# Kernel optimization log

Hardware: AMD Instinct MI355X
Metric: run time of the kernel (lower is better)

## Reference

```python
import jax, jax.numpy as jnp
import numpy as np
from jax import lax
from jax.scipy.linalg import cho_solve, solve_triangular

T_LEN, D, K = 8192, 32, 16
LOG2PI = float(np.log(2.0 * np.pi))


def setup_inputs():
    ks = jax.random.split(jax.random.key(0), 14)
    R = 0.1 * jax.random.normal(ks[0], (T_LEN, D, D))
    recog_J = jnp.einsum('tij,tkj->tik', R, R) + 0.5 * jnp.eye(D)  # SPD recognition precisions
    recog_h = 0.1 * jax.random.normal(ks[1], (T_LEN, D, 1))
    loc = 0.1 * jax.random.normal(ks[2], (D, 1))
    Tau_p = jnp.eye(D) + 0.05 * jax.random.normal(ks[3], (D, D))
    Lambda_p = jnp.eye(D) + 0.05 * jax.random.normal(ks[4], (D, D))
    X = 0.9 * jnp.eye(D, D + 1) + 0.05 * jax.random.normal(ks[5], (D, D + 1))
    init_lps = jax.nn.log_softmax(jax.random.normal(ks[6], (K,)))[:, None]
    trans_lps = jax.nn.log_softmax(jax.random.normal(ks[7], (K, K)), axis=1)
    Rp = 0.1 * jax.random.normal(ks[8], (K, D, D))
    prior_lam = jnp.einsum('kij,klj->kil', Rp, Rp) + jnp.eye(D)
    prior_X = 0.9 * jnp.eye(D, D + 1) + 0.05 * jax.random.normal(ks[9], (K, D, D + 1))
    Rt = 0.1 * jax.random.normal(ks[10], (D, D))
    prior_tau = Rt @ Rt.T + jnp.eye(D)
    prior_mu = 0.1 * jax.random.normal(ks[11], (D, 1))
    init_lps_prior = jax.nn.log_softmax(jax.random.normal(ks[12], (K,)))[:, None]
    trans_lps_prior = jax.nn.log_softmax(jax.random.normal(ks[13], (K, K)), axis=1)
    return dict(recog_J=recog_J, recog_h=recog_h, loc=loc, Tau_p=Tau_p, Lambda_p=Lambda_p, X=X,
                init_lps=init_lps, trans_lps=trans_lps, prior_lam=prior_lam, prior_X=prior_X,
                prior_tau=prior_tau, prior_mu=prior_mu, init_lps_prior=init_lps_prior,
                trans_lps_prior=trans_lps_prior, seed=42)


def _slds(recog_J, recog_h, loc, Tau_p, Lambda_p, X, init_lps, trans_lps,
          prior_lam, prior_X, prior_tau, prior_mu, init_lps_prior, trans_lps_prior, seed):
    Dd = loc.shape[0]
    Kk = init_lps.shape[0]
    Tt = recog_J.shape[0]
    Nn = Tt - 1
    eye = jnp.eye(Dd, dtype=recog_J.dtype)
    jitter = 1e-6 * eye

    # expected_params: inference LDS natural params
    tau = Tau_p @ Tau_p.T + 1e-8 * eye
    tau_mu = tau @ loc
    lam = Lambda_p @ Lambda_p.T + 1e-8 * eye
    A = X[:, :Dd]
    b = X[:, Dd:]
    ATlam = A.T @ lam
    ATlamA = ATlam @ A
    lamA = lam @ A
    lamb = lam @ b
    ATlamb = A.T @ lamb
    bTlamb = (b.T @ lamb)[0, 0]
    logdet_lam = jnp.linalg.slogdet(lam)[1]

    # ---- HMM forward-backward over z_{1:N} (emissions are zeros, kept general) ----
    emit = jnp.zeros((Nn, Kk), dtype=recog_J.dtype)

    def fstep(a, e):
        a2 = jax.nn.logsumexp(a[:, None] + trans_lps, axis=0) + e
        return a2, a2
    a0 = init_lps[:, 0] + emit[0]
    _, alphas_rest = lax.scan(fstep, a0, emit[1:])
    alphas = jnp.concatenate([a0[None], alphas_rest], 0)  # (N,K)
    hmm_logZ = jax.nn.logsumexp(alphas[-1])

    def bstep(beta_next, e_next):
        beta = jax.nn.logsumexp(trans_lps + (e_next + beta_next)[None, :], axis=1)
        return beta, beta
    _, betas_head = lax.scan(bstep, jnp.zeros(Kk, dtype=recog_J.dtype), emit[1:], reverse=True)
    betas = jnp.concatenate([betas_head, jnp.zeros((1, Kk), dtype=recog_J.dtype)], 0)
    cat_es = jnp.exp(alphas + betas - hmm_logZ)  # (N,K) marginals q(z_t)
    pair = jnp.exp(alphas[:-1, :, None] + trans_lps[None] + (emit[1:] + betas[1:])[:, None, :] - hmm_logZ)
    EZZNT = jnp.sum(pair, 0)  # (K,K) expected transition counts

    hmm_kl = (jnp.sum(cat_es[0] * (init_lps[:, 0] - init_lps_prior[:, 0]))
              + jnp.sum(EZZNT * (trans_lps - trans_lps_prior))
              + jnp.sum(cat_es * emit) - hmm_logZ)

    # ---- LDS information-form Kalman filter (computes logZ of q) ----
    J0 = tau + recog_J[0]
    h0 = tau_mu + recog_h[0]
    logc0 = -0.5 * (loc.T @ tau_mu)[0, 0] + 0.5 * jnp.linalg.slogdet(tau)[1] - 0.5 * Dd * LOG2PI

    def filt(carry, xs):
        J, h, lc = carry
        Jr, hr = xs
        M = J + ATlamA + jitter
        C = jnp.linalg.cholesky(M)
        u = h - ATlamb
        Minv_u = cho_solve((C, True), u)
        logdetM = 2.0 * jnp.sum(jnp.log(jnp.diagonal(C)))
        Jn = lam + Jr - lamA @ cho_solve((C, True), ATlam)
        hn = lamb + hr + lamA @ Minv_u
        lc = lc - 0.5 * bTlamb + 0.5 * logdet_lam + 0.5 * (u.T @ Minv_u)[0, 0] - 0.5 * logdetM
        return (Jn, hn, lc), (Jn, hn)

    (Jlast, hlast, logc), (Jf_rest, hf_rest) = lax.scan(filt, (J0, h0, logc0), (recog_J[1:], recog_h[1:]))
    Jf = jnp.concatenate([J0[None], Jf_rest], 0)  # (T,D,D) filtered precisions
    hf = jnp.concatenate([h0[None], hf_rest], 0)  # (T,D,1)
    Cl = jnp.linalg.cholesky(Jlast + jitter)
    mlast = cho_solve((Cl, True), hlast)
    logZq = logc + 0.5 * (hlast.T @ mlast)[0, 0] + 0.5 * Dd * LOG2PI - jnp.sum(jnp.log(jnp.diagonal(Cl)))

    # ---- RTS smoother -> gaussian expected stats ----
    CovT = cho_solve((Cl, True), eye)

    def smooth(carry, xs):
        m_n, Cov_n = carry
        Jt, ht = xs
        P = Jt + ATlamA + jitter
        C = jnp.linalg.cholesky(P)
        G = cho_solve((C, True), ATlam)
        g = cho_solve((C, True), ht - ATlamb)
        m = G @ m_n + g
        Pinv = cho_solve((C, True), eye)
        Cov = Pinv + G @ Cov_n @ G.T
        cross = G @ (Cov_n + m_n @ m_n.T) + g @ m_n.T  # E[x_t x_{t+1}^T]
        return (m, Cov), (m, Cov, cross)

    _, (m_head, Cov_head, cross) = lax.scan(smooth, (mlast, CovT), (Jf[:-1], hf[:-1]), reverse=True)
    Ex = jnp.concatenate([m_head, mlast[None]], 0)  # (T,D,1)
    Cov = jnp.concatenate([Cov_head, CovT[None]], 0)
    ExxT = Cov + jnp.einsum('tiz,tjz->tij', Ex, Ex)  # (T,D,D)
    Cross = jnp.swapaxes(cross, 1, 2)  # E[x_{t+1} x_t^T], (N,D,D)
    Ex2 = Ex[..., 0]

    # ---- E_q[log p_inf(x)] ----
    init_term = (-0.5 * jnp.einsum('ij,ij->', tau, ExxT[0]) + jnp.dot(Ex2[0], tau_mu[:, 0])
                 - 0.5 * (loc.T @ tau_mu)[0, 0] + 0.5 * jnp.linalg.slogdet(tau)[1] - 0.5 * Dd * LOG2PI)
    trans_term = (-0.5 * jnp.einsum('ij,nij->', lam, ExxT[1:])
                  + jnp.einsum('ij,nij->', lamA, Cross)
                  - 0.5 * jnp.einsum('ij,nij->', ATlamA, ExxT[:-1])
                  + jnp.einsum('i,ni->', lamb[:, 0], Ex2[1:])
                  - jnp.einsum('i,ni->', ATlamb[:, 0], Ex2[:-1])
                  + Nn * (-0.5 * bTlamb + 0.5 * logdet_lam - 0.5 * Dd * LOG2PI))
    E_log_p_inf = init_term + trans_term

    # ---- hmm_to_lds_mf: mixture (mean-field) prior expected log-density ----
    Ak = prior_X[:, :, :Dd]
    bk = prior_X[:, :, Dd:]
    lamAk = jnp.einsum('kij,kjl->kil', prior_lam, Ak)
    ATlamAk = jnp.einsum('kji,kjl->kil', Ak, lamAk)
    lambk = jnp.einsum('kij,kjz->kiz', prior_lam, bk)
    ATlambk = jnp.einsum('kji,kjz->kiz', Ak, lambk)
    bTlambk = jnp.einsum('kjz,kjz->k', bk, lambk)
    logdetk = jnp.linalg.slogdet(prior_lam)[1]
    w = cat_es  # (N,K)
    mix_trans = (-0.5 * jnp.einsum('nk,kij,nij->', w, prior_lam, ExxT[1:])
                 + jnp.einsum('nk,kij,nij->', w, lamAk, Cross)
                 - 0.5 * jnp.einsum('nk,kij,nij->', w, ATlamAk, ExxT[:-1])
                 + jnp.einsum('nk,ki,ni->', w, lambk[:, :, 0], Ex2[1:])
                 - jnp.einsum('nk,ki,ni->', w, ATlambk[:, :, 0], Ex2[:-1])
                 + jnp.einsum('nk,k->', w, -0.5 * bTlambk + 0.5 * logdetk)
                 - 0.5 * Nn * Dd * LOG2PI)
    tpm = prior_tau @ prior_mu
    mix_init = (-0.5 * jnp.einsum('ij,ij->', prior_tau, ExxT[0]) + jnp.dot(Ex2[0], tpm[:, 0])
                - 0.5 * (prior_mu.T @ tpm)[0, 0] + 0.5 * jnp.linalg.slogdet(prior_tau)[1] - 0.5 * Dd * LOG2PI)
    E_log_p_mix = mix_init + mix_trans

    recog_term = (-0.5 * jnp.einsum('tij,tij->', recog_J, ExxT)
                  + jnp.einsum('tiz,tiz->', recog_h, Ex))
    lds_kl = E_log_p_inf + recog_term - logZq - E_log_p_mix

    # ---- joint backward sampling of x_{1:T} ~ q ----
    eps = jax.random.normal(jax.random.fold_in(jax.random.key(seed), 1), (Tt, Dd, 1), dtype=recog_J.dtype)
    xT = mlast + solve_triangular(Cl.T, eps[-1], lower=False)

    def samp(x_next, xs):
        Jt, ht, e = xs
        P = Jt + ATlamA + jitter
        C = jnp.linalg.cholesky(P)
        mean = cho_solve((C, True), ht - ATlamb + ATlam @ x_next)
        x = mean + solve_triangular(C.T, e, lower=False)
        return x, x

    _, xs_head = lax.scan(samp, xT, (Jf[:-1], hf[:-1], eps[:-1]), reverse=True)
    z = jnp.concatenate([xs_head, xT[None]], 0)[..., 0]  # (T,D)

    return z, Ex, ExxT, Cross, cat_es, lds_kl + hmm_kl


def reference(recog_J, recog_h, loc, Tau_p, Lambda_p, X, init_lps, trans_lps,
              prior_lam, prior_X, prior_tau, prior_mu, init_lps_prior, trans_lps_prior, seed):
    return _slds(recog_J, recog_h, loc, Tau_p, Lambda_p, X, init_lps, trans_lps,
                 prior_lam, prior_X, prior_tau, prior_mu, init_lps_prior, trans_lps_prior, seed)
```

## Files before the change

kernel.cpp:

```cpp
#include <hip/hip_runtime.h>
#include <math.h>
#include <stdint.h>

#define Dd 32
#define TT 8192
#define NN 8191
#define KK 16
#define LOG2PI_ 1.8378770664093453

#define WSD_LOGC0  0
#define WSD_LOGZQ  1
#define WSD_MIXC   3
#define WSD_LDLAM  4
#define WSD_BTLAMB 5
#define WSD_PR     8
#define WSD_PT     1032
#define WSD_PM     2056
#define F_TAU      0
#define F_TAUMU    1024
#define F_LAM      1056
#define F_A        2080
#define F_B        3104
#define F_ATLAM    3136
#define F_ATLAMA   4160
// ... 121 lines not shown
  dst[(j0+2)*36+m]=v.z; dst[(j0+3)*36+m]=v.w;
}
__device__ __forceinline__ void t36_sym(float* dst, const float* packed, int tid){
  for(int q=tid;q<528;q+=256){
    int r,c; tri_rc(q,r,c);
    float v=packed[q];
    dst[r*36+c]=v; dst[c*36+r]=v;
  }
}

__device__ double chol_linv36(float* W, float* Li, float* rdg, int tid){
  int r = tid>>3, c0 = (tid&7)<<2;
  {
    float4 z = make_float4(0.f,0.f,0.f,0.f);
    if(r>=c0 && r<c0+4) ((float*)&z)[r-c0]=1.f;
    *(float4*)(Li + r*36 + c0) = z;
  }
  double slog=0.0;
  for(int j=0;j<33;++j){
    if(j<32){
      float dd = W[j*36+j];
      float rd = 1.0f/sqrtf(dd);
      float invd = rd*rd;
      if(tid==0){ rdg[j]=rd; slog += (double)(0.5f*__logf(dd)); }
      if(r>j && c0+3>=j){
        float t0 = W[j*36+r]*invd;
        float4 wj  = *(const float4*)(W+j*36+c0);
        float4 cur = *(float4*)(W+r*36+c0);
        float rdl = rd;
        int c;
        c=c0;   cur.x = (c>j)? fmaf(-t0, wj.x, cur.x) : ((c==j)? cur.x*rdl : cur.x);
        c=c0+1; cur.y = (c>j)? fmaf(-t0, wj.y, cur.y) : ((c==j)? cur.y*rdl : cur.y);
        c=c0+2; cur.z = (c>j)? fmaf(-t0, wj.z, cur.z) : ((c==j)? cur.z*rdl : cur.z);
        c=c0+3; cur.w = (c>j)? fmaf(-t0, wj.w, cur.w) : ((c==j)? cur.w*rdl : cur.w);
        *(float4*)(W+r*36+c0) = cur;
      }
    }
    if(j>0){
      int ii=j-1;
      if(r>ii && c0<=ii){
        float wri = W[r*36+ii]*rdg[ii];
        float4 lrow = *(const float4*)(Li+ii*36+c0);
        float4 cur  = *(float4*)(Li+r*36+c0);
        if(c0+0<=ii) cur.x = fmaf(-wri, lrow.x, cur.x);
        if(c0+1<=ii) cur.y = fmaf(-wri, lrow.y, cur.y);
        if(c0+2<=ii) cur.z = fmaf(-wri, lrow.z, cur.z);
        if(c0+3<=ii) cur.w = fmaf(-wri, lrow.w, cur.w);
        *(float4*)(Li+r*36+c0) = cur;
      }
    }
    __syncthreads();
  }
  {
    float rr = rdg[r];
    float4 cur = *(float4*)(Li+r*36+c0);
    cur.x*=rr; cur.y*=rr; cur.z*=rr; cur.w*=rr;
    *(float4*)(Li+r*36+c0) = cur;
  }
  __syncthreads();
  return slog;
}

__device__ __forceinline__ double blk_red(double v, double* sd, int tid){
  sd[tid]=v; __syncthreads();
  for(int s=128;s>0;s>>=1){ if(tid<s) sd[tid]+=sd[tid+s]; __syncthreads(); }
  double r=sd[0]; __syncthreads(); return r;
}
__device__ double blk_logdet(float* Ms, int tid){
  double sl = 0.0;
  for (int j=0;j<Dd;++j){
    float dd = Ms[j*33+j];
    sl += log((double)dd);
    float invd = 1.0f/dd;
    #pragma unroll
    for(int p=0;p<4;p++){
      int cell = tid + (p<<8); int r=cell>>5, c=cell&31;
      if(r>j && c>j && c<=r) Ms[r*33+c] -= Ms[r*33+j]*(Ms[c*33+j]*invd);
    }
    __syncthreads();
  }
  return sl;
}

__global__ __launch_bounds__(256) void k_setup(const float* rJ, const float* rh, const float* loc,
    const float* Tp, const float* Lp, const float* X, const float* plam, const float* pX,
    const float* ptau, const float* pmu, float* wsf, double* wsd){
  __shared__ float s1[1056], s2[1056], s3[1056];
  __shared__ float sv[32], sv2[32];
  int tid=threadIdx.x; int b=blockIdx.x;
  if(b==0){
    for(int p=0;p<4;p++){int cell=tid+(p<<8);int r=cell>>5,c=cell&31; s1[r*33+c]=Tp[cell];}
    if(tid<32) sv[tid]=loc[tid];
    __syncthreads();
    for(int p=0;p<4;p++){int cell=tid+(p<<8);int r=cell>>5,c=cell&31;
      float a=0.f;
      #pragma unroll
      for(int m=0;m<Dd;++m) a=fmaf(s1[r*33+m], s1[c*33+m], a);
      if(r==c) a+=1e-8f;
      s2[r*33+c]=a; wsf[F_TAU+cell]=a; wsf[F_J0+cell]=a+rJ[cell];
    }
    __syncthreads();
    if(tid<32){ float tm=0.f;
      #pragma unroll
      for(int m=0;m<Dd;++m) tm=fmaf(s2[tid*33+m], sv[m], tm);
      sv2[tid]=tm; wsf[F_TAUMU+tid]=tm; wsf[F_H0+tid]=tm+rh[tid];
    }
    __syncthreads();
    double ldt = blk_logdet(s2, tid);
    if(tid==0){ double dd=0; for(int m=0;m<Dd;++m) dd += (double)sv[m]*(double)sv2[m];
      wsd[WSD_LOGC0] = -0.5*dd + 0.5*ldt - 0.5*Dd*LOG2PI_; }
  } else if(b==1){
    for(int p=0;p<4;p++){int cell=tid+(p<<8);int r=cell>>5,c=cell&31; s1[r*33+c]=Lp[cell];}
    __syncthreads();
    for(int p=0;p<4;p++){int cell=tid+(p<<8);int r=cell>>5,c=cell&31;
      float a=0.f;
      #pragma unroll
      for(int m=0;m<Dd;++m) a=fmaf(s1[r*33+m], s1[c*33+m], a);
      if(r==c) a+=1e-8f;
      s2[r*33+c]=a; wsf[F_LAM+cell]=a;
    }
    __syncthreads();
    for(int p=0;p<4;p++){int cell=tid+(p<<8);int r=cell>>5,c=cell&31;
      float a=X[r*33+c]; s3[r*33+c]=a; wsf[F_A+cell]=a; }
    if(tid<32){ sv[tid]=X[tid*33+32]; wsf[F_B+tid]=sv[tid]; }
    __syncthreads();
    for(int p=0;p<4;p++){int cell=tid+(p<<8);int r=cell>>5,c=cell&31;
      float a=0.f,b2=0.f;
      #pragma unroll
      for(int m=0;m<Dd;++m){ a=fmaf(s2[r*33+m], s3[m*33+c], a); b2=fmaf(s3[m*33+r], s2[m*33+c], b2); }
      s1[r*33+c]=a; wsf[F_LAMA+cell]=a; wsf[F_ATLAM+cell]=b2;
    }
    if(tid<32){ float lb=0.f;
      #pragma unroll
      for(int m=0;m<Dd;++m) lb=fmaf(s2[tid*33+m], sv[m], lb);
      sv2[tid]=lb; wsf[F_LAMB+tid]=lb;
    }
    __syncthreads();
    for(int p=0;p<4;p++){int cell=tid+(p<<8);int r=cell>>5,c=cell&31;
      float a=0.f;
      #pragma unroll
      for(int m=0;m<Dd;++m) a=fmaf(s3[m*33+r], s1[m*33+c], a);
      wsf[F_ATLAMA+cell]=a;
    }
    if(tid<32){ float ab=0.f;
      #pragma unroll
      for(int m=0;m<Dd;++m) ab=fmaf(s3[m*33+tid], sv2[m], ab);
      wsf[F_ATLAMB+tid]=ab;
    }
    if(tid==0){ double bb=0; for(int m=0;m<Dd;++m) bb += (double)sv[m]*(double)sv2[m];
      wsd[WSD_BTLAMB]=bb; }
    __syncthreads();
    double ldl = blk_logdet(s2, tid);
    if(tid==0) wsd[WSD_LDLAM]=ldl;
  } else if(b==2){
    for(int p=0;p<4;p++){int cell=tid+(p<<8);int r=cell>>5,c=cell&31; s1[r*33+c]=ptau[cell];}
    if(tid<32) sv[tid]=pmu[tid];
    __syncthreads();
    if(tid<32){ float tm=0.f;
      #pragma unroll
      for(int m=0;m<Dd;++m) tm=fmaf(s1[tid*33+m], sv[m], tm);
      sv2[tid]=tm; wsf[F_TPM+tid]=tm;
    }
    __syncthreads();
    double ldp = blk_logdet(s1, tid);
    if(tid==0){ double dd=0; for(int m=0;m<Dd;++m) dd += (double)sv[m]*(double)sv2[m];
      wsd[WSD_MIXC] = -0.5*dd + 0.5*ldp - 0.5*Dd*LOG2PI_; }
// ... 68 lines not shown

__global__ __launch_bounds__(256) void k_hmmab(const float* il, float* wsf){
  __shared__ float S[3328];
  int tid=threadIdx.x;
  for(int p=0;p<13;++p) S[p*256+tid]=wsf[F_TPOW+p*256+tid];
  __syncthreads();
  int n = blockIdx.x*256 + tid;
  if(n>NN-1) return;
  float v[16], w[16];
  #pragma unroll
  for(int j=0;j<16;++j) v[j]=il[j];
  for(int k=0;k<13;++k){
    if((n>>k)&1){
      #pragma unroll
      for(int j=0;j<16;++j){
        float mx=-3.0e38f;
        #pragma unroll
        for(int i2=0;i2<16;++i2) mx=fmaxf(mx, v[i2]+S[k*256+i2*16+j]);
        float s=0.f;
        #pragma unroll
        for(int i2=0;i2<16;++i2) s+=__expf(v[i2]+S[k*256+i2*16+j]-mx);
        w[j]=mx+__logf(s);
      }
      #pragma unroll
      for(int j=0;j<16;++j) v[j]=w[j];
    }
  }
  #pragma unroll
  for(int j=0;j<16;++j) wsf[F_ALPHA+(size_t)n*16+j]=v[j];
  if(n==NN-1){
    float mx=-3.0e38f;
    #pragma unroll
    for(int j=0;j<16;++j) mx=fmaxf(mx,v[j]);
    float s=0.f;
    #pragma unroll
    for(int j=0;j<16;++j) s+=__expf(v[j]-mx);
    wsf[F_SC+0]=mx+__logf(s);
  }
  int m = NN-1-n;
  float b[16];
  #pragma unroll
  for(int i2=0;i2<16;++i2) b[i2]=0.f;
  for(int k=0;k<13;++k){
    if((m>>k)&1){
      #pragma unroll
      for(int i2=0;i2<16;++i2){
        float mx=-3.0e38f;
        #pragma unroll
        for(int j=0;j<16;++j) mx=fmaxf(mx, S[k*256+i2*16+j]+b[j]);
        float s=0.f;
        #pragma unroll
        for(int j=0;j<16;++j) s+=__expf(S[k*256+i2*16+j]+b[j]-mx);
        w[i2]=mx+__logf(s);
      }
      #pragma unroll
      for(int i2=0;i2<16;++i2) b[i2]=w[i2];
    }
  }
  #pragma unroll
  for(int i2=0;i2<16;++i2) wsf[F_BETA+(size_t)n*16+i2]=b[i2];
}

__global__ __launch_bounds__(256) void k_cat(const float* tl, float* wsf, float* out){
  __shared__ float Ts[256]; __shared__ float al[1024]; __shared__ float be[1040];
  int tid=threadIdx.x;
  Ts[tid]=tl[tid];
  float logZ = wsf[F_SC+0];
  int n0=blockIdx.x*64;
  for(int q=tid;q<1024;q+=256){ int n=n0+(q>>4); al[q] = (n<NN)? wsf[F_ALPHA+(size_t)n*16+(q&15)] : 0.f; }
  for(int q=tid;q<1040;q+=256){ int n=n0+(q>>4); be[q] = (n<NN)? wsf[F_BETA +(size_t)n*16+(q&15)] : 0.f; }
  __syncthreads();
  for(int q=tid;q<1024;q+=256){ int n=n0+(q>>4);
    if(n<NN) out[O_CAT+(size_t)n*16+(q&15)] = __expf(al[q]+be[q]-logZ); }
  int i=tid>>4, j=tid&15;
  float acc=0.f;
  #pragma unroll 4
  for(int nn=0;nn<64;++nn){
    int n=n0+nn;
    if(n<NN-1) acc += __expf(al[nn*16+i]+Ts[i*16+j]+be[(nn+1)*16+j]-logZ);
  }
  wsf[F_EZ + blockIdx.x*256 + tid]=acc;
}

__global__ __launch_bounds__(256) void k_leaf(const float* rJ, const float* rh, float* wsf, double* wsd){
  int b = blockIdx.x; int tid=threadIdx.x;
  float* pe = wsf + F_SCAN + (size_t)b*SSTR;
  if(b==0){
    for(int q=tid;q<528;q+=256){
      int r,c; tri_rc(q,r,c);
      pe[POFF+q]=0.f;
      pe[QOFF+q]=wsf[F_J0 + r*32+c];
    }
    for(int q=tid;q<1024;q+=256) pe[ROFF+q]=0.f;
    if(tid<32){ pe[PPOFF+tid]=0.f; pe[QQOFF+tid]=wsf[F_H0+tid]; }
    if(tid==0){ *(double*)(pe+GAMOFF)=wsd[WSD_LOGC0]; pe[FLGOFF]=1.f; }
  } else {
    int t = b;
    for(int q=tid;q<528;q+=256){
      int r,c; tri_rc(q,r,c);
      pe[POFF+q] = wsf[F_ATLAMA + r*32+c] + ((r==c)?1e-6f:0.f);
      pe[QOFF+q] = wsf[F_LAM + r*32+c] + rJ[(size_t)t*1024 + r*32+c];
    }
    for(int q=tid;q<1024;q+=256) pe[ROFF+q] = -wsf[F_ATLAM+q];
    if(tid<32){
      pe[PPOFF+tid] = -wsf[F_ATLAMB+tid];
      pe[QQOFF+tid] = wsf[F_LAMB+tid] + rh[(size_t)t*32+tid];
    }
    if(tid==0){
      *(double*)(pe+GAMOFF) = -0.5*wsd[WSD_BTLAMB] + 0.5*wsd[WSD_LDLAM];
      pe[FLGOFF]=1.f;
    }
  }
}

__global__ __launch_bounds__(256) void k_cf(float* wsf, float* out, int d, int mode){
  __shared__ __align__(16) float SA[2148], SB[2148];
  __shared__ __align__(16) float W[1152], Li[1152], BA[1152], BB[1152];
  __shared__ float rdg[32], Ls[32];
  int tid = threadIdx.x;
  int i = blockIdx.x;
  int iA = (i<<(d+1)) + (1<<d) - 1;
  int iB = iA + (1<<d);
  float* base = wsf + F_SCAN;
  float* pa = base + (size_t)iA*SSTR;
  float* pb = base + (size_t)iB*SSTR;
  for(int q=tid;q<537;q+=256){ ((float4*)SA)[q]=((const float4*)pa)[q]; ((float4*)SB)[q]=((const float4*)pb)[q]; }
  __syncthreads();
  int fa=(SA[FLGOFF]!=0.f), fb=(SB[FLGOFF]!=0.f);
  if(mode==1){
    float* st = out + O_EXXT;
    for(int q=tid;q<537;q+=256){ ((float4*)st)[q]=((float4*)SB)[q]; ((float4*)pb)[q]=((float4*)SA)[q]; }
    if(tid==0) pa[FLGOFF]=0.f;
    return;
  }
  if(mode==2){ for(int q=tid;q<537;q+=256) ((float4*)pa)[q]=((float4*)SB)[q]; }
  float* X = (mode==2)? SB : SA;  int fx=(mode==2)?fb:fa;
  float* Y = (mode==2)? SA : SB;  int fy=(mode==2)?fa:fb;
  if(!fx && !fy){ if(tid==0) pb[FLGOFF]=0.f; return; }
  if(!fx){ for(int q=tid;q<537;q+=256) ((float4*)pb)[q]=((float4*)Y)[q]; return; }
  if(!fy){ for(int q=tid;q<537;q+=256) ((float4*)pb)[q]=((float4*)X)[q]; return; }
  for(int q=tid;q<528;q+=256){
    int r,c; tri_rc(q,r,c);
    float w = X[QOFF+q] + Y[POFF+q];
    W[r*36+c]=w; W[c*36+r]=w;
  }
  t36_rows(BA, X+ROFF, tid);
  t36_tr  (BB, Y+ROFF, tid);
  __syncthreads();
  double slog = chol_linv36(W, Li, rdg, tid);
  if(tid<32){
    float acc=0.f;
    for(int m=0;m<=tid;++m) acc = fmaf(Li[tid*36+m], X[QQOFF+m]+Y[PPOFF+m], acc);
    Ls[tid]=acc;
  }
  for(int q=tid;q<1024;q+=256){
    int i2=q>>5, j=q&31;
    W[j*36+i2] = dot36(Li, i2, BA, j);
  }
  __syncthreads();
  for(int q=tid;q<1024;q+=256){
    int i2=q>>5, j=q&31;
    BA[j*36+i2] = dot36(Li, i2, BB, j);
  }
  __syncthreads();
  for(int q=tid;q<528;q+=256){
    int r,c; tri_rc(q,r,c);
    pb[POFF+q] = X[POFF+q] - dot36(W, r, W, c);
    pb[QOFF+q] = Y[QOFF+q] - dot36(BA, r, BA, c);
  }
  for(int q=tid;q<1024;q+=256){
    int r=q>>5, c=q&31;
    pb[ROFF+q] = -dot36(W, r, BA, c);
  }
  if(tid<32){
    float ap=0.f,aq=0.f;
    #pragma unroll
    for(int m=0;m<32;++m){ ap=fmaf(W[tid*36+m],Ls[m],ap); aq=fmaf(BA[tid*36+m],Ls[m],aq); }
    pb[PPOFF+tid] = X[PPOFF+tid] - ap;
    pb[QQOFF+tid] = Y[QQOFF+tid] - aq;
  }
  if(tid==0){
    double g = *(double*)(X+GAMOFF) + *(double*)(Y+GAMOFF);
    double dot=0.0;
    for(int m=0;m<32;++m) dot += (double)Ls[m]*(double)Ls[m];
    *(double*)(pb+GAMOFF) = g + 0.5*dot - slog;
    pb[FLGOFF]=1.f;
  }
}

__global__ __launch_bounds__(256) void k_point(float* wsf, double* wsd, float* out){
  __shared__ __align__(16) float SE[2148];
  __shared__ __align__(16) float W[1152], Li[1152], AUX[1152];
  __shared__ float rdg[32], uv[32], Lu[32], ev[32], gv[32], yv[32];
  int tid=threadIdx.x; int b=blockIdx.x;
  float* base = wsf + F_SCAN;
  float* outz = out + O_Z;
  if(b>0){
    int t = b-1;
    float* pe = base + (size_t)b*SSTR;
    for(int q=tid;q<537;q+=256) ((float4*)SE)[q]=((const float4*)pe)[q];
    if(tid<32) ev[tid]=outz[(size_t)t*32+tid];
    t36_rows(AUX, wsf+F_LAMA, tid);
    __syncthreads();
    for(int q=tid;q<528;q+=256){
      int r,c; tri_rc(q,r,c);
      float w = SE[QOFF+q] + wsf[F_ATLAMA + r*32+c] + ((r==c)?1e-6f:0.f);
      W[r*36+c]=w; W[c*36+r]=w;
    }
    if(tid<32) uv[tid]=SE[QQOFF+tid]-wsf[F_ATLAMB+tid];
    __syncthreads();
    chol_linv36(W, Li, rdg, tid);
    if(tid<32){
      float acc=0.f;
      for(int m=0;m<=tid;++m) acc=fmaf(Li[tid*36+m],uv[m],acc);
      Lu[tid]=acc;
    }
    for(int q=tid;q<1024;q+=256){
      int i2=q>>5, j=q&31;
      W[j*36+i2] = dot36(Li, i2, AUX, j);
    }
    __syncthreads();
    t36_tr36(AUX, Li, tid);
    if(tid<32){
      float ag=0.f, ay=0.f;
      for(int m2=tid;m2<32;++m2){ float lv=Li[m2*36+tid]; ag=fmaf(lv,Lu[m2],ag); ay=fmaf(lv,ev[m2],ay); }
      gv[tid]=ag; yv[tid]=ay;
    }
    __syncthreads();
    for(int q=tid;q<1024;q+=256){
      int r=q>>5,c=q&31;
      pe[BG+q] = dot36(AUX, r, W, c);
    }
    float* outc = out + O_CROSS + (size_t)t*1024;
    for(int q=tid;q<528;q+=256){
      int r,c; tri_rc(q,r,c);
      float a = dot36(AUX, r, AUX, c);
      pe[BP+q]=a; outc[q]=a;
    }
    if(tid<32){
      pe[BCM+tid]=gv[tid]; pe[BCZ+tid]=gv[tid]+yv[tid]; outc[528+tid]=gv[tid];
    }
    if(tid==0) pe[FLGOFF]=1.f;
  } else {
    const float* st = out + O_EXXT;
    for(int q=tid;q<537;q+=256) ((float4*)SE)[q]=((const float4*)st)[q];
    if(tid<32) ev[tid]=outz[(size_t)NN*32+tid];
    __syncthreads();
    for(int q=tid;q<528;q+=256){
      int r,c; tri_rc(q,r,c);
      float w = SE[QOFF+q] + ((r==c)?1e-6f:0.f);
      W[r*36+c]=w; W[c*36+r]=w;
    }
    if(tid<32) uv[tid]=SE[QQOFF+tid];
    __syncthreads();
    double slog2 = chol_linv36(W, Li, rdg, tid);
    if(tid<32){
      float acc=0.f;
      for(int m=0;m<=tid;++m) acc=fmaf(Li[tid*36+m],uv[m],acc);
      Lu[tid]=acc;
    }
    t36_tr36(AUX, Li, tid);
    __syncthreads();
    if(tid<32){
      float am=0.f, ay=0.f;
      for(int m2=tid;m2<32;++m2){ float lv=Li[m2*36+tid]; am=fmaf(lv,Lu[m2],am); ay=fmaf(lv,ev[m2],ay); }
      gv[tid]=am; yv[tid]=ay;
      wsf[F_MLAST+tid]=am; out[O_EX+(size_t)NN*32+tid]=am;
      float xt=am+ay;
      wsf[F_XT+tid]=xt; out[O_Z+(size_t)NN*32+tid]=xt;
    }
    __syncthreads();
    for(int q=tid;q<1024;q+=256){
      int r=q>>5,c=q&31;
      float a = dot36(AUX, r, AUX, c);
      wsf[F_COVT+q]=a;
      out[O_EXXT+(size_t)NN*1024+q]=a+gv[r]*gv[c];
    }
    if(tid==0){
      double gam=*(const double*)(SE+GAMOFF);
      double hm=0.0;
      for(int m=0;m<32;++m) hm += (double)uv[m]*(double)gv[m];
      wsd[WSD_LOGZQ] = gam + 0.5*hm + 0.5*Dd*LOG2PI_ - slog2;
    }
  }
}

__device__ __forceinline__ int amap(int j){ return (j<NN)? (NN-j) : 0; }

__global__ __launch_bounds__(256) void k_ca(float* wsf, int d, int mode){
  __shared__ __align__(16) float SA[2148], SB[2148];
  __shared__ __align__(16) float GY36[1152], GB[1152], PX36[1152];
  int tid = threadIdx.x;
  int i = blockIdx.x;
  int iA = (i<<(d+1)) + (1<<d) - 1;
  int iB = iA + (1<<d);
  float* base = wsf + F_SCAN;
  float* pa = base + (size_t)amap(iA)*SSTR;
  float* pb = base + (size_t)amap(iB)*SSTR;
  for(int q=tid;q<537;q+=256){ ((float4*)SA)[q]=((const float4*)pa)[q]; ((float4*)SB)[q]=((const float4*)pb)[q]; }
  __syncthreads();
  int fa=(SA[FLGOFF]!=0.f), fb=(SB[FLGOFF]!=0.f);
  if(mode==1){
    for(int q=tid;q<537;q+=256) ((float4*)pb)[q]=((float4*)SA)[q];
    if(tid==0) pa[FLGOFF]=0.f;
    return;
  }
  if(mode==2){ for(int q=tid;q<537;q+=256) ((float4*)pa)[q]=((float4*)SB)[q]; }
  float* X = (mode==2)? SB : SA;  int fx=(mode==2)?fb:fa;
  float* Y = (mode==2)? SA : SB;  int fy=(mode==2)?fa:fb;
  if(!fx && !fy){ if(tid==0) pb[FLGOFF]=0.f; return; }
  if(!fx){ for(int q=tid;q<537;q+=256) ((float4*)pb)[q]=((float4*)Y)[q]; return; }
  if(!fy){ for(int q=tid;q<537;q+=256) ((float4*)pb)[q]=((float4*)X)[q]; return; }
  t36_rows(GY36, Y+BG, tid);
  t36_tr  (GB,   X+BG, tid);
  t36_sym (PX36, X+BP, tid);
  __syncthreads();
  for(int q=tid;q<1024;q+=256){
    int r=q>>5,c=q&31;
    pb[BG+q] = dot36(GY36, r, GB, c);
  }
  __syncthreads();
  for(int q=tid;q<1024;q+=256){
    int r=q>>5,c=q&31;
    GB[r*36+c] = dot36(GY36, r, PX36, c);
  }
  __syncthreads();
  for(int q=tid;q<528;q+=256){
    int r,c; tri_rc(q,r,c);
    pb[BP+q] = dot36(GB, r, GY36, c) + Y[BP+q];
  }
  if(tid<32){
    float az=0.f,am=0.f;
    #pragma unroll
    for(int m=0;m<32;++m){ float g=GY36[tid*36+m]; az=fmaf(g,X[BCZ+m],az); am=fmaf(g,X[BCM+m],am); }
    pb[BCZ+tid]=az+Y[BCZ+tid];
    pb[BCM+tid]=am+Y[BCM+tid];
  }
  if(tid==0) pb[FLGOFF]=1.f;
}

__global__ __launch_bounds__(256) void k_smz(float* wsf, float* out){
  __shared__ __align__(16) float G36[1152], CV36[1152], Tm36[1152];
  __shared__ float mlv[32], xtv[32], mv[32], zv[32];
  int tid=threadIdx.x;
  int t = blockIdx.x;
  const float* pe = wsf + F_SCAN + (size_t)t*SSTR;
  t36_rows(G36,  pe+BG,       tid);
  t36_rows(CV36, wsf+F_COVT,  tid);
  if(tid<32){ mlv[tid]=wsf[F_MLAST+tid]; xtv[tid]=wsf[F_XT+tid]; }
  __syncthreads();
  if(tid<32){
    float am=0.f, az=0.f;
    #pragma unroll
    for(int m=0;m<32;++m){
      float g=G36[tid*36+m];
      am=fmaf(g, mlv[m], am);
      az=fmaf(g, xtv[m], az);
    }
    mv[tid]=am+pe[BCM+tid];
    zv[tid]=az+pe[BCZ+tid];
    out[O_EX+(size_t)t*32+tid]=mv[tid];
    out[O_Z +(size_t)t*32+tid]=zv[tid];
  }
  for(int q=tid;q<1024;q+=256){
    int r=q>>5,c=q&31;
    Tm36[r*36+c] = dot36(G36, r, CV36, c);
  }
  __syncthreads();
  for(int q=tid;q<528;q+=256){
    int r,c; tri_rc(q,r,c);
    float cov = dot36(Tm36, r, G36, c) + pe[BP+q];
    float e = cov + mv[r]*mv[c];
    out[O_EXXT+(size_t)t*1024 + r*32+c]=e;
    if(r!=c) out[O_EXXT+(size_t)t*1024 + c*32+r]=e;
  }
}

__global__ __launch_bounds__(256) void k_cross(float* wsf, float* out){
  __shared__ __align__(16) float PV36[1152], LA36[1152], E136[1152], GF36[1152];
  __shared__ float gv[32], m1[32];
  int tid=threadIdx.x;
  int t = blockIdx.x;
  float* outc = out + O_CROSS + (size_t)t*1024;
  t36_sym (PV36, outc, tid);
  t36_rows(LA36, wsf+F_LAMA, tid);
  t36_rows(E136, out+O_EXXT+(size_t)(t+1)*1024, tid);
  if(tid<32){ gv[tid]=outc[528+tid]; m1[tid]=out[O_EX+(size_t)(t+1)*32+tid]; }
  __syncthreads();
  for(int q=tid;q<1024;q+=256){
    int r=q>>5,c=q&31;
    GF36[r*36+c] = dot36(PV36, r, LA36, c);
  }
  __syncthreads();
  for(int q=tid;q<1024;q+=256){
    int i2=q>>5, j=q&31;
    float acc = dot36(GF36, j, E136, i2);
    outc[q] = acc + gv[j]*m1[i2];
  }
}

__global__ __launch_bounds__(256) void k_terms(const float* rJ, const float* rh,
    const float* plam, float* wsf, double* wsd, float* out){
  __shared__ float slam[1056], slamA[1056], sata[1056];
  __shared__ float slamb[32], satlb[32], cst[16], sw[16];
  __shared__ double sd[256];
  int tid=threadIdx.x; int i8=tid>>3, c4=(tid&7)*4;
  for(int p=0;p<4;p++){int cell=tid+(p<<8);int r=cell>>5,c=cell&31;
    slam[r*33+c]=wsf[F_LAM+cell]; slamA[r*33+c]=wsf[F_LAMA+cell]; sata[r*33+c]=wsf[F_ATLAMA+cell];}
  if(tid<32){slamb[tid]=wsf[F_LAMB+tid]; satlb[tid]=wsf[F_ATLAMB+tid];}
  if(tid<16) cst[tid] = -0.5f*wsf[F_BTLAMBK+tid] + 0.5f*wsf[F_LOGDETK+tid];
  __syncthreads();
  double dr=0.0, dt=0.0, dm=0.0;
  int t0=blockIdx.x*8;
  for(int tt=0;tt<8;++tt){
    int t=t0+tt;
    if(t<NN){ if(tid<16) sw[tid]=out[O_CAT+(size_t)t*16+tid]; }
    __syncthreads();
    size_t cb=(size_t)t*1024+((size_t)i8<<5)+c4;
    float4 exT=*(const float4*)(out+O_EXXT+cb);
    float4 rj =*(const float4*)(rJ+cb);
    dr += -0.5*(double)(rj.x*exT.x+rj.y*exT.y+rj.z*exT.z+rj.w*exT.w);
    if(tid<32) dr += (double)(rh[(size_t)t*32+tid]*out[O_EX+(size_t)t*32+tid]);
    if(t>=1){
      dt += -0.5*(double)(slam[i8*33+c4]*exT.x + slam[i8*33+c4+1]*exT.y
                        + slam[i8*33+c4+2]*exT.z + slam[i8*33+c4+3]*exT.w);
      if(tid<32) dt += (double)(slamb[tid]*out[O_EX+(size_t)t*32+tid]);
    }
    if(t<NN){
      float4 crT =*(const float4*)(out+O_CROSS+cb);
      float4 exT1=*(const float4*)(out+O_EXXT+cb+1024);
      dt += (double)(slamA[i8*33+c4]*crT.x + slamA[i8*33+c4+1]*crT.y
                   + slamA[i8*33+c4+2]*crT.z + slamA[i8*33+c4+3]*crT.w)
          -0.5*(double)(sata[i8*33+c4]*exT.x + sata[i8*33+c4+1]*exT.y
                      + sata[i8*33+c4+2]*exT.z + sata[i8*33+c4+3]*exT.w);
      if(tid<32) dt -= (double)(satlb[tid]*out[O_EX+(size_t)t*32+tid]);
      const float* pe1=(const float*)&exT1; const float* pcr=(const float*)&crT; const float* pe0=(const float*)&exT;
      #pragma unroll
      for(int q=0;q<4;q++){
        int cc=(i8<<5)+c4+q;
        float wl=0.f, wa=0.f, wt2=0.f;
        #pragma unroll
        for(int k2=0;k2<KK;k2++){ float wv=sw[k2];
          wl =fmaf(wv, plam[(size_t)k2*1024+cc], wl);
          wa =fmaf(wv, wsf[F_LAMAK+(size_t)k2*1024+cc], wa);
          wt2=fmaf(wv, wsf[F_ATLAMAK+(size_t)k2*1024+cc], wt2);}
        dm += (double)(-0.5f*wl*pe1[q] + wa*pcr[q] - 0.5f*wt2*pe0[q]);
      }
      if(tid<32){
        float wlb=0.f, wtb=0.f;
        #pragma unroll
        for(int k2=0;k2<KK;k2++){ wlb=fmaf(sw[k2], wsf[F_LAMBK+k2*32+tid], wlb);
                                  wtb=fmaf(sw[k2], wsf[F_ATLAMBK+k2*32+tid], wtb);}
        dm += (double)(wlb*out[O_EX+(size_t)(t+1)*32+tid] - wtb*out[O_EX+(size_t)t*32+tid]);
      }
      if(tid<16) dm += (double)(sw[tid]*cst[tid]);
    }
    __syncthreads();
  }
  double r1=blk_red(dr,sd,tid);
  double r2=blk_red(dt,sd,tid);
  double r3=blk_red(dm,sd,tid);
  if(tid==0){ wsd[WSD_PR+blockIdx.x]=r1; wsd[WSD_PT+blockIdx.x]=r2; wsd[WSD_PM+blockIdx.x]=r3; }
}

__global__ __launch_bounds__(256) void k_final(const float* il, const float* tl,
    const float* ilp, const float* tlp, const float* ptau, float* wsf, double* wsd, float* out){
  __shared__ double sd[256];
  int tid=threadIdx.x;
  double ez=0.0;
  for(int b=0;b<128;++b) ez += (double)wsf[F_EZ + b*256 + tid];
  double v = ez * (double)(tl[tid]-tlp[tid]);
  if(tid<16) v += (double)out[O_CAT+tid] * (double)(il[tid]-ilp[tid]);
  double hmmkl = blk_red(v, sd, tid) - (double)wsf[F_SC+0];
  double a=0,b2=0,c=0;
  for(int q=0;q<4;q++){int b3=tid+q*256; a+=wsd[WSD_PR+b3]; b2+=wsd[WSD_PT+b3]; c+=wsd[WSD_PM+b3];}
  double recog=blk_red(a,sd,tid), trns=blk_red(b2,sd,tid), mixt=blk_red(c,sd,tid);
  double ia=0, ib=0, va=0, vb=0;
  for(int p=0;p<4;p++){int cell=tid+(p<<8);
    float e0=out[O_EXXT+cell];
    ia += (double)(wsf[F_TAU+cell]*e0);
    ib += (double)(ptau[cell]*e0);
  }
  if(tid<32){ float ex0=out[O_EX+tid];
    va=(double)(ex0*wsf[F_TAUMU+tid]); vb=(double)(ex0*wsf[F_TPM+tid]); }
  double s_ia=blk_red(ia,sd,tid), s_ib=blk_red(ib,sd,tid);
  double s_va=blk_red(va,sd,tid), s_vb=blk_red(vb,sd,tid);
  if(tid==0){
    double init_term = -0.5*s_ia + s_va + wsd[WSD_LOGC0];
    double mix_init  = -0.5*s_ib + s_vb + wsd[WSD_MIXC];
    double trans_term = trns + (double)NN*(-0.5*wsd[WSD_BTLAMB] + 0.5*wsd[WSD_LDLAM] - 0.5*Dd*LOG2PI_);
    double mix_trans  = mixt - 0.5*(double)NN*(double)Dd*LOG2PI_;
    double lds_kl = (init_term+trans_term) + recog - wsd[WSD_LOGZQ] - (mix_init+mix_trans);
    out[O_KL] = (float)(lds_kl + hmmkl);
  }
}

extern "C" void kernel_launch(void* const* d_in, const int* in_sizes, int n_in,
                              void* d_out, int out_size, void* d_ws, size_t ws_size,
                              hipStream_t stream){
  const float* rJ  =(const float*)d_in[0];
  const float* rh  =(const float*)d_in[1];
  const float* loc =(const float*)d_in[2];
  const float* Tp  =(const float*)d_in[3];
  const float* Lp  =(const float*)d_in[4];
  const float* X   =(const float*)d_in[5];
  const float* il  =(const float*)d_in[6];
  const float* tl  =(const float*)d_in[7];
  const float* plam=(const float*)d_in[8];
  const float* pX  =(const float*)d_in[9];
  const float* ptau=(const float*)d_in[10];
  const float* pmu =(const float*)d_in[11];
  const float* ilp =(const float*)d_in[12];
  const float* tlp =(const float*)d_in[13];
  const int*   seed=(const int*)d_in[14];
  float* out=(float*)d_out;
  double* wsd=(double*)d_ws;
  float* wsf=(float*)((char*)d_ws + 32768);

  k_setup<<<19,256,0,stream>>>(rJ,rh,loc,Tp,Lp,X,plam,pX,ptau,pmu,wsf,wsd);
  k_eps<<<1024,256,0,stream>>>(seed, out + O_Z);
  k_hmmpow<<<1,256,0,stream>>>(tl, wsf);
  k_hmmab<<<32,256,0,stream>>>(il, wsf);
  k_cat<<<128,256,0,stream>>>(tl, wsf, out);
  k_leaf<<<8192,256,0,stream>>>(rJ, rh, wsf, wsd);
  for(int d=0; d<13; ++d) k_cf<<<(8192>>(d+1)),256,0,stream>>>(wsf, out, d, 0);
  k_cf<<<1,256,0,stream>>>(wsf, out, 12, 1);
  for(int d=11; d>=0; --d) k_cf<<<(8192>>(d+1)),256,0,stream>>>(wsf, out, d, 2);
  k_point<<<8192,256,0,stream>>>(wsf, wsd, out);
  for(int d=0; d<13; ++d) k_ca<<<(8192>>(d+1)),256,0,stream>>>(wsf, d, 0);
  k_ca<<<1,256,0,stream>>>(wsf, 12, 1);
  for(int d=11; d>=0; --d) k_ca<<<(8192>>(d+1)),256,0,stream>>>(wsf, d, 2);
  k_smz<<<NN,256,0,stream>>>(wsf, out);
  k_cross<<<NN,256,0,stream>>>(wsf, out);
  k_terms<<<1024,256,0,stream>>>(rJ, rh, plam, wsf, wsd, out);
  k_final<<<1,256,0,stream>>>(il, tl, ilp, tlp, ptau, wsf, wsd, out);
}
```

Before: 2.043 ms.

## Fuse leaf element generation into first scan level and tune occupancy

Removes the separate k_leaf kernel. The d==0 level of the Cholesky-scan kernel now builds the leaf elements directly in shared memory from the inputs, rather than reading them back from the workspace. In mode 2 at d==0, leaf A is regenerated the same way. It also adds minimum-blocks-per-CU launch bounds to several scan and smoothing kernels, plus unroll pragmas on the strided loops. The intent is to drop one full write-then-read of the per-timestep workspace and to raise occupancy, at the risk of register spills from the tighter launch bounds.

```diff
diff --git a/kernel.cpp b/kernel.cpp
--- a/kernel.cpp
+++ b/kernel.cpp
@@ -227,6 +227,39 @@
   return sl;
 }
 
+__device__ void gen_leaf(float* S, int s, const float* rJ, const float* rh,
+                         const float* wsf, const double* wsd, int tid){
+  if(s==0){
+    #pragma unroll 3
+    for(int q=tid;q<528;q+=256){
+      int r,c; tri_rc(q,r,c);
+      S[POFF+q]=0.f;
+      S[QOFF+q]=wsf[F_J0 + r*32+c];
+    }
+    #pragma unroll 4
+    for(int q=tid;q<1024;q+=256) S[ROFF+q]=0.f;
+    if(tid<32){ S[PPOFF+tid]=0.f; S[QQOFF+tid]=wsf[F_H0+tid]; }
+    if(tid==0){ *(double*)(S+GAMOFF)=wsd[WSD_LOGC0]; S[FLGOFF]=1.f; }
+  } else {
+    #pragma unroll 3
+    for(int q=tid;q<528;q+=256){
+      int r,c; tri_rc(q,r,c);
+      S[POFF+q] = wsf[F_ATLAMA + r*32+c] + ((r==c)?1e-6f:0.f);
+      S[QOFF+q] = wsf[F_LAM + r*32+c] + rJ[(size_t)s*1024 + r*32+c];
+    }
+    #pragma unroll 4
+    for(int q=tid;q<1024;q+=256) S[ROFF+q] = -wsf[F_ATLAM+q];
+    if(tid<32){
+      S[PPOFF+tid] = -wsf[F_ATLAMB+tid];
+      S[QQOFF+tid] = wsf[F_LAMB+tid] + rh[(size_t)s*32+tid];
+    }
+    if(tid==0){
+      *(double*)(S+GAMOFF) = -0.5*wsd[WSD_BTLAMB] + 0.5*wsd[WSD_LDLAM];
+      S[FLGOFF]=1.f;
+    }
+  }
+}
+
 __global__ __launch_bounds__(256) void k_setup(const float* rJ, const float* rh, const float* loc,
     const float* Tp, const float* Lp, const float* X, const float* plam, const float* pX,
     const float* ptau, const float* pmu, float* wsf, double* wsd){
@@ -461,38 +494,8 @@
   wsf[F_EZ + blockIdx.x*256 + tid]=acc;
 }
 
-__global__ __launch_bounds__(256) void k_leaf(const float* rJ, const float* rh, float* wsf, double* wsd){
-  int b = blockIdx.x; int tid=threadIdx.x;
-  float* pe = wsf + F_SCAN + (size_t)b*SSTR;
-  if(b==0){
-    for(int q=tid;q<528;q+=256){
-      int r,c; tri_rc(q,r,c);
-      pe[POFF+q]=0.f;
-      pe[QOFF+q]=wsf[F_J0 + r*32+c];
-    }
-    for(int q=tid;q<1024;q+=256) pe[ROFF+q]=0.f;
-    if(tid<32){ pe[PPOFF+tid]=0.f; pe[QQOFF+tid]=wsf[F_H0+tid]; }
-    if(tid==0){ *(double*)(pe+GAMOFF)=wsd[WSD_LOGC0]; pe[FLGOFF]=1.f; }
-  } else {
-    int t = b;
-    for(int q=tid;q<528;q+=256){
-      int r,c; tri_rc(q,r,c);
-      pe[POFF+q] = wsf[F_ATLAMA + r*32+c] + ((r==c)?1e-6f:0.f);
-      pe[QOFF+q] = wsf[F_LAM + r*32+c] + rJ[(size_t)t*1024 + r*32+c];
-    }
-    for(int q=tid;q<1024;q+=256) pe[ROFF+q] = -wsf[F_ATLAM+q];
-    if(tid<32){
-      pe[PPOFF+tid] = -wsf[F_ATLAMB+tid];
-      pe[QQOFF+tid] = wsf[F_LAMB+tid] + rh[(size_t)t*32+tid];
-    }
-    if(tid==0){
-      *(double*)(pe+GAMOFF) = -0.5*wsd[WSD_BTLAMB] + 0.5*wsd[WSD_LDLAM];
-      pe[FLGOFF]=1.f;
-    }
-  }
-}
-
-__global__ __launch_bounds__(256) void k_cf(float* wsf, float* out, int d, int mode){
+__global__ __launch_bounds__(256,4) void k_cf(const float* rJ, const float* rh,
+    float* wsf, double* wsd, float* out, int d, int mode){
   __shared__ __align__(16) float SA[2148], SB[2148];
   __shared__ __align__(16) float W[1152], Li[1152], BA[1152], BB[1152];
   __shared__ float rdg[32], Ls[32];
@@ -503,21 +506,40 @@
   float* base = wsf + F_SCAN;
   float* pa = base + (size_t)iA*SSTR;
   float* pb = base + (size_t)iB*SSTR;
-  for(int q=tid;q<537;q+=256){ ((float4*)SA)[q]=((const float4*)pa)[q]; ((float4*)SB)[q]=((const float4*)pb)[q]; }
+  if(d==0){
+    gen_leaf(SA, iA, rJ, rh, wsf, wsd, tid);
+    if(mode==0) gen_leaf(SB, iB, rJ, rh, wsf, wsd, tid);
+    else { 
+      #pragma unroll 3
+      for(int q=tid;q<537;q+=256) ((float4*)SB)[q]=((const float4*)pb)[q];
+    }
+  } else {
+    #pragma unroll 3
+    for(int q=tid;q<537;q+=256){ ((float4*)SA)[q]=((const float4*)pa)[q]; ((float4*)SB)[q]=((const float4*)pb)[q]; }
+  }
   __syncthreads();
   int fa=(SA[FLGOFF]!=0.f), fb=(SB[FLGOFF]!=0.f);
   if(mode==1){
     float* st = out + O_EXXT;
+    #pragma unroll 3
     for(int q=tid;q<537;q+=256){ ((float4*)st)[q]=((float4*)SB)[q]; ((float4*)pb)[q]=((float4*)SA)[q]; }
     if(tid==0) pa[FLGOFF]=0.f;
     return;
   }
-  if(mode==2){ for(int q=tid;q<537;q+=256) ((float4*)pa)[q]=((float4*)SB)[q]; }
+  if(mode==2){
+    #pragma unroll 3
+    for(int q=tid;q<537;q+=256) ((float4*)pa)[q]=((float4*)SB)[q];
+  }
   float* X = (mode==2)? SB : SA;  int fx=(mode==2)?fb:fa;
   float* Y = (mode==2)? SA : SB;  int fy=(mode==2)?fa:fb;
   if(!fx && !fy){ if(tid==0) pb[FLGOFF]=0.f; return; }
-  if(!fx){ for(int q=tid;q<537;q+=256) ((float4*)pb)[q]=((float4*)Y)[q]; return; }
-  if(!fy){ for(int q=tid;q<537;q+=256) ((float4*)pb)[q]=((float4*)X)[q]; return; }
+  if(!fx){ 
+    #pragma unroll 3
+    for(int q=tid;q<537;q+=256) ((float4*)pb)[q]=((float4*)Y)[q]; return; }
+  if(!fy){ 
+    #pragma unroll 3
+    for(int q=tid;q<537;q+=256) ((float4*)pb)[q]=((float4*)X)[q]; return; }
+  #pragma unroll 3
   for(int q=tid;q<528;q+=256){
     int r,c; tri_rc(q,r,c);
     float w = X[QOFF+q] + Y[POFF+q];
@@ -532,21 +554,25 @@
     for(int m=0;m<=tid;++m) acc = fmaf(Li[tid*36+m], X[QQOFF+m]+Y[PPOFF+m], acc);
     Ls[tid]=acc;
   }
+  #pragma unroll 4
   for(int q=tid;q<1024;q+=256){
     int i2=q>>5, j=q&31;
     W[j*36+i2] = dot36(Li, i2, BA, j);
   }
   __syncthreads();
+  #pragma unroll 4
   for(int q=tid;q<1024;q+=256){
     int i2=q>>5, j=q&31;
     BA[j*36+i2] = dot36(Li, i2, BB, j);
   }
   __syncthreads();
+  #pragma unroll 3
   for(int q=tid;q<528;q+=256){
     int r,c; tri_rc(q,r,c);
     pb[POFF+q] = X[POFF+q] - dot36(W, r, W, c);
     pb[QOFF+q] = Y[QOFF+q] - dot36(BA, r, BA, c);
   }
+  #pragma unroll 4
   for(int q=tid;q<1024;q+=256){
     int r=q>>5, c=q&31;
     pb[ROFF+q] = -dot36(W, r, BA, c);
@@ -567,7 +593,7 @@
   }
 }
 
-__global__ __launch_bounds__(256) void k_point(float* wsf, double* wsd, float* out){
+__global__ __launch_bounds__(256,6) void k_point(float* wsf, double* wsd, float* out){
   __shared__ __align__(16) float SE[2148];
   __shared__ __align__(16) float W[1152], Li[1152], AUX[1152];
   __shared__ float rdg[32], uv[32], Lu[32], ev[32], gv[32], yv[32];
@@ -577,10 +603,12 @@
   if(b>0){
     int t = b-1;
     float* pe = base + (size_t)b*SSTR;
+    #pragma unroll 3
     for(int q=tid;q<537;q+=256) ((float4*)SE)[q]=((const float4*)pe)[q];
     if(tid<32) ev[tid]=outz[(size_t)t*32+tid];
     t36_rows(AUX, wsf+F_LAMA, tid);
     __syncthreads();
+    #pragma unroll 3
     for(int q=tid;q<528;q+=256){
       int r,c; tri_rc(q,r,c);
       float w = SE[QOFF+q] + wsf[F_ATLAMA + r*32+c] + ((r==c)?1e-6f:0.f);
@@ -594,6 +622,7 @@
       for(int m=0;m<=tid;++m) acc=fmaf(Li[tid*36+m],uv[m],acc);
       Lu[tid]=acc;
     }
+    #pragma unroll 4
     for(int q=tid;q<1024;q+=256){
       int i2=q>>5, j=q&31;
       W[j*36+i2] = dot36(Li, i2, AUX, j);
@@ -606,11 +635,13 @@
       gv[tid]=ag; yv[tid]=ay;
     }
     __syncthreads();
+    #pragma unroll 4
     for(int q=tid;q<1024;q+=256){
       int r=q>>5,c=q&31;
       pe[BG+q] = dot36(AUX, r, W, c);
     }
     float* outc = out + O_CROSS + (size_t)t*1024;
+    #pragma unroll 3
     for(int q=tid;q<528;q+=256){
       int r,c; tri_rc(q,r,c);
       float a = dot36(AUX, r, AUX, c);
@@ -622,6 +653,7 @@
     if(tid==0) pe[FLGOFF]=1.f;
   } else {
     const float* st = out + O_EXXT;
+    #pragma unroll 3
     for(int q=tid;q<537;q+=256) ((float4*)SE)[q]=((const float4*)st)[q];
     if(tid<32) ev[tid]=outz[(size_t)NN*32+tid];
     __syncthreads();
@@ -666,7 +698,7 @@
 
 __device__ __forceinline__ int amap(int j){ return (j<NN)? (NN-j) : 0; }
 
-__global__ __launch_bounds__(256) void k_ca(float* wsf, int d, int mode){
+__global__ __launch_bounds__(256,4) void k_ca(float* wsf, int d, int mode){
   __shared__ __align__(16) float SA[2148], SB[2148];
   __shared__ __align__(16) float GY36[1152], GB[1152], PX36[1152];
   int tid = threadIdx.x;
@@ -676,34 +708,46 @@
   float* base = wsf + F_SCAN;
   float* pa = base + (size_t)amap(iA)*SSTR;
   float* pb = base + (size_t)amap(iB)*SSTR;
+  #pragma unroll 3
   for(int q=tid;q<537;q+=256){ ((float4*)SA)[q]=((const float4*)pa)[q]; ((float4*)SB)[q]=((const float4*)pb)[q]; }
   __syncthreads();
   int fa=(SA[FLGOFF]!=0.f), fb=(SB[FLGOFF]!=0.f);
   if(mode==1){
+    #pragma unroll 3
     for(int q=tid;q<537;q+=256) ((float4*)pb)[q]=((float4*)SA)[q];
     if(tid==0) pa[FLGOFF]=0.f;
     return;
   }
-  if(mode==2){ for(int q=tid;q<537;q+=256) ((float4*)pa)[q]=((float4*)SB)[q]; }
+  if(mode==2){
+    #pragma unroll 3
+    for(int q=tid;q<537;q+=256) ((float4*)pa)[q]=((float4*)SB)[q];
+  }
   float* X = (mode==2)? SB : SA;  int fx=(mode==2)?fb:fa;
   float* Y = (mode==2)? SA : SB;  int fy=(mode==2)?fa:fb;
   if(!fx && !fy){ if(tid==0) pb[FLGOFF]=0.f; return; }
-  if(!fx){ for(int q=tid;q<537;q+=256) ((float4*)pb)[q]=((float4*)Y)[q]; return; }
-  if(!fy){ for(int q=tid;q<537;q+=256) ((float4*)pb)[q]=((float4*)X)[q]; return; }
+  if(!fx){ 
+    #pragma unroll 3
+    for(int q=tid;q<537;q+=256) ((float4*)pb)[q]=((float4*)Y)[q]; return; }
+  if(!fy){ 
+    #pragma unroll 3
+    for(int q=tid;q<537;q+=256) ((float4*)pb)[q]=((float4*)X)[q]; return; }
   t36_rows(GY36, Y+BG, tid);
   t36_tr  (GB,   X+BG, tid);
   t36_sym (PX36, X+BP, tid);
   __syncthreads();
+  #pragma unroll 4
   for(int q=tid;q<1024;q+=256){
     int r=q>>5,c=q&31;
     pb[BG+q] = dot36(GY36, r, GB, c);
   }
   __syncthreads();
+  #pragma unroll 4
   for(int q=tid;q<1024;q+=256){
     int r=q>>5,c=q&31;
     GB[r*36+c] = dot36(GY36, r, PX36, c);
   }
   __syncthreads();
+  #pragma unroll 3
   for(int q=tid;q<528;q+=256){
     int r,c; tri_rc(q,r,c);
     pb[BP+q] = dot36(GB, r, GY36, c) + Y[BP+q];
@@ -718,7 +762,7 @@
   if(tid==0) pb[FLGOFF]=1.f;
 }
 
-__global__ __launch_bounds__(256) void k_smz(float* wsf, float* out){
+__global__ __launch_bounds__(256,6) void k_smz(float* wsf, float* out){
   __shared__ __align__(16) float G36[1152], CV36[1152], Tm36[1152];
   __shared__ float mlv[32], xtv[32], mv[32], zv[32];
   int tid=threadIdx.x;
@@ -741,11 +785,13 @@
     out[O_EX+(size_t)t*32+tid]=mv[tid];
     out[O_Z +(size_t)t*32+tid]=zv[tid];
   }
+  #pragma unroll 4
   for(int q=tid;q<1024;q+=256){
     int r=q>>5,c=q&31;
     Tm36[r*36+c] = dot36(G36, r, CV36, c);
   }
   __syncthreads();
+  #pragma unroll 3
   for(int q=tid;q<528;q+=256){
     int r,c; tri_rc(q,r,c);
     float cov = dot36(Tm36, r, G36, c) + pe[BP+q];
@@ -755,7 +801,7 @@
   }
 }
 
-__global__ __launch_bounds__(256) void k_cross(float* wsf, float* out){
+__global__ __launch_bounds__(256,6) void k_cross(float* wsf, float* out){
   __shared__ __align__(16) float PV36[1152], LA36[1152], E136[1152], GF36[1152];
   __shared__ float gv[32], m1[32];
   int tid=threadIdx.x;
@@ -766,11 +812,13 @@
   t36_rows(E136, out+O_EXXT+(size_t)(t+1)*1024, tid);
   if(tid<32){ gv[tid]=outc[528+tid]; m1[tid]=out[O_EX+(size_t)(t+1)*32+tid]; }
   __syncthreads();
+  #pragma unroll 4
   for(int q=tid;q<1024;q+=256){
     int r=q>>5,c=q&31;
     GF36[r*36+c] = dot36(PV36, r, LA36, c);
   }
   __syncthreads();
+  #pragma unroll 4
   for(int q=tid;q<1024;q+=256){
     int i2=q>>5, j=q&31;
     float acc = dot36(GF36, j, E136, i2);
@@ -901,10 +949,9 @@
   k_hmmpow<<<1,256,0,stream>>>(tl, wsf);
   k_hmmab<<<32,256,0,stream>>>(il, wsf);
   k_cat<<<128,256,0,stream>>>(tl, wsf, out);
-  k_leaf<<<8192,256,0,stream>>>(rJ, rh, wsf, wsd);
-  for(int d=0; d<13; ++d) k_cf<<<(8192>>(d+1)),256,0,stream>>>(wsf, out, d, 0);
-  k_cf<<<1,256,0,stream>>>(wsf, out, 12, 1);
-  for(int d=11; d>=0; --d) k_cf<<<(8192>>(d+1)),256,0,stream>>>(wsf, out, d, 2);
+  for(int d=0; d<13; ++d) k_cf<<<(8192>>(d+1)),256,0,stream>>>(rJ, rh, wsf, wsd, out, d, 0);
+  k_cf<<<1,256,0,stream>>>(rJ, rh, wsf, wsd, out, 12, 1);
+  for(int d=11; d>=0; --d) k_cf<<<(8192>>(d+1)),256,0,stream>>>(rJ, rh, wsf, wsd, out, d, 2);
   k_point<<<8192,256,0,stream>>>(wsf, wsd, out);
   for(int d=0; d<13; ++d) k_ca<<<(8192>>(d+1)),256,0,stream>>>(wsf, d, 0);
   k_ca<<<1,256,0,stream>>>(wsf, 12, 1);
```

Result: no change. 2.077 ms (+1.6%).
